# Optimization experiments

Hardware: AMD Instinct MI355X
Metric: run time of the kernel (lower is better)

## Reference

```python
import jax, jax.numpy as jnp
import numpy as np

NEG = -1e30  # safe -inf surrogate (keeps grads finite)
BLANK = 0
PRIOR_SCALE = 0.3


def prior_logsumexp(log_probs, input_lengths):
    # log_probs: [T, N, V]; logsumexp over all valid (t, n) frames -> [1, V]
    T = log_probs.shape[0]
    mask = jnp.arange(T)[:, None] < input_lengths[None, :]  # [T, N]
    masked = jnp.where(mask[:, :, None], log_probs, NEG)
    return jax.nn.logsumexp(masked, axis=(0, 1))[None, :]


def ctc_loss_mean(log_probs, targets, input_lengths, target_lengths):
    # Exact CTC forward (alpha) recursion, vectorized over batch, scanned over time.
    # log_probs: [T, N, V] (log scores), targets: [N, S] with values >= 1.
    T, N, V = log_probs.shape
    S = targets.shape[1]
    L = 2 * S + 1  # extended label sequence with interleaved blanks
    ext = jnp.full((N, L), BLANK, dtype=targets.dtype).at[:, 1::2].set(targets)
    # skip transition j-2 -> j allowed iff ext[j] != blank and ext[j] != ext[j-2]
    skip = jnp.zeros((N, L), bool).at[:, 2:].set(
        (ext[:, 2:] != BLANK) & (ext[:, 2:] != ext[:, :-2]))
    pad1 = jnp.full((N, 1), NEG, log_probs.dtype)
    pad2 = jnp.full((N, 2), NEG, log_probs.dtype)

    e0 = jnp.take_along_axis(log_probs[0], ext, axis=1)  # [N, L]
    alpha0 = (jnp.full((N, L), NEG, log_probs.dtype)
              .at[:, 0].set(e0[:, 0])
              .at[:, 1].set(e0[:, 1]))

    def step(alpha, xs):
        lp_t, t = xs
        emit = jnp.take_along_axis(lp_t, ext, axis=1)  # [N, L]
        s1 = jnp.concatenate([pad1, alpha[:, :-1]], axis=1)
        s2 = jnp.where(skip, jnp.concatenate([pad2, alpha[:, :-2]], axis=1), NEG)
        new = jax.nn.logsumexp(jnp.stack([alpha, s1, s2], 0), axis=0) + emit
        # freeze finished utterances (t >= input_length)
        alpha = jnp.where((t < input_lengths)[:, None], new, alpha)
        return alpha, None

    alpha, _ = jax.lax.scan(step, alpha0, (log_probs[1:], jnp.arange(1, T)))

    i1 = (2 * target_lengths)[:, None]
    a1 = jnp.take_along_axis(alpha, i1, axis=1)[:, 0]
    a2 = jnp.take_along_axis(alpha, i1 - 1, axis=1)[:, 0]
    ll = jnp.logaddexp(a1, a2)  # total log-likelihood per utterance
    # k2.ctc_loss(reduction='mean', target_lengths=...) == mean of (-ll / target_len)
    return jnp.mean(-ll / target_lengths.astype(log_probs.dtype))


def setup_inputs() -> dict:
    key = jax.random.key(0)
    k1, k2, k3, k4, k5 = jax.random.split(key, 5)
    T, N, V, S = 2000, 32, 256, 256
    log_probs = jax.nn.log_softmax(jax.random.normal(k1, (T, N, V), jnp.float32), axis=-1)
    log_priors = jax.nn.log_softmax(0.5 * jax.random.normal(k2, (1, V), jnp.float32), axis=-1)
    targets = jax.random.randint(k3, (N, S), 1, V)          # non-blank labels
    input_lengths = jax.random.randint(k4, (N,), T // 2, T + 1)
    target_lengths = jax.random.randint(k5, (N,), S // 2, S + 1)
    return {"log_probs": log_probs, "log_priors": log_priors, "targets": targets,
            "input_lengths": input_lengths, "target_lengths": target_lengths}


def reference(log_probs, log_priors, targets, input_lengths, target_lengths):
    # (1) detached label-prior accumulation pass (as in training step)
    log_batch_priors_sum = jax.lax.stop_gradient(prior_logsumexp(log_probs, input_lengths))
    # (2) prior-scaled log probs (log_priors broadcasts [1,V] -> [T,N,V])
    scaled = log_probs - PRIOR_SCALE * log_priors
    # (3) CTC forward-backward loss
    loss = ctc_loss_mean(scaled, targets, input_lengths, target_lengths)
    return loss, log_batch_priors_sum
```

## Files before the change

kernel.cpp:

```cpp
#include <hip/hip_runtime.h>

#define PRIOR_SCALE 0.3f
#define NEGF (-1e30f)
#define LOG2E_F 1.4426950408889634f
#define LN2_F 0.6931471805599453f
#define K_SS 8
#define MARG 24

#define PHASE_BARRIER() \
  asm volatile("s_waitcnt lgkmcnt(0)\n\ts_barrier" ::: "memory")

__device__ __forceinline__ float fexp2(float x) { return __builtin_amdgcn_exp2f(x); }
__device__ __forceinline__ float flog2(float x) { return __builtin_amdgcn_logf(x); }

__device__ __forceinline__ float lse2b(float a, float b) {
  float m = fmaxf(a, b);
  float d = fminf(a, b) - m;
  return m + flog2(1.0f + fexp2(d));
}

__device__ __forceinline__ float shr1_dpp(float x, float fill) {
  return __int_as_float(__builtin_amdgcn_update_dpp(
      __float_as_int(fill), __float_as_int(x), 0x138 , 0xF, 0xF, false));
}
__device__ __forceinline__ int shr1_dpp_i(int x, int fill) {
  return __builtin_amdgcn_update_dpp(fill, x, 0x138, 0xF, 0xF, false);
}
template <int CTRL, int RM>
__device__ __forceinline__ int dppi(int x) {
  return __builtin_amdgcn_update_dpp(x, x, CTRL, RM, 0xF, false);
}
__device__ __forceinline__ int imax2(int a, int b) { return a > b ? a : b; }

__device__ __forceinline__ void issue_pair(float& e, float& b, uint32_t offE,
                                           uint32_t offB, uint64_t base) {
  asm volatile("global_load_dword %0, %2, %4\n\t"
               "global_load_dword %1, %3, %4"
               : "=v"(e), "=v"(b)
               : "v"(offE), "v"(offB), "s"(base));
}
__device__ __forceinline__ void wait_pair(float& e, float& b) {
  asm volatile("s_waitcnt vmcnt(14)" : "+v"(e), "+v"(b));
}

extern "C" __global__ void __launch_bounds__(256, 1)
ctc_fused_kernel(const float* __restrict__ lp, const float* __restrict__ lpri,
                 const int* __restrict__ tgt, const int* __restrict__ ilen,
                 const int* __restrict__ tlen, float* __restrict__ nll,
                 float* __restrict__ partial, int pblocks,
                 int T, int N, int V, int S) {
  if ((int)blockIdx.x >= N) {
    const int pb = blockIdx.x - N;
    const int v = threadIdx.x;
    float s = 0.0f;
    for (int t = pb; t < T; t += pblocks) {
      const float* base = lp + (size_t)t * N * V + v;
      for (int nn = 0; nn < N; ++nn) {
        float x = base[(size_t)nn * V];
        s += (t < ilen[nn]) ? __expf(x) : 0.0f;
      }
    }
    partial[(size_t)pb * V + v] = s;
    return;
  }

  const int n = blockIdx.x;
  const int g = threadIdx.x;
  const int lane = g & 63;
  const int wid = __builtin_amdgcn_readfirstlane(threadIdx.x >> 6);
  __shared__ __align__(16) float mb[3][2048];
  __shared__ int mbe[3][256];
  __shared__ float afin[513];

  const int len = __builtin_amdgcn_readfirstlane(ilen[n]);
  const int tl = tlen[n];

  const int* trow = tgt + n * S;
  const int tv = trow[g];
  const int tvp = (g > 0) ? trow[g - 1] : -1;
  const float skf = (g > 0 && tv != tvp) ? 1.0f : 0.0f;
  const float ep1 = (-PRIOR_SCALE * lpri[tv]) * LOG2E_F;
  const float epb = (-PRIOR_SCALE * lpri[0]) * LOG2E_F;
  const int penB = MARG * ((lane & 15) + 1);
  const int penC = MARG * ((lane & 31) + 1);

  const float* rp = lp + (size_t)n * V;
  const uint32_t RBu = (uint32_t)(N * V * 4);
  const uint32_t tvb = (uint32_t)tv * 4u;
  const uint64_t gbase = (uint64_t)(uintptr_t)rp;

  float x0 = 0.0f, x1 = 0.0f, x2 = 0.0f;
  int e = 0;
  { float b0 = rp[0], e0 = rp[tv];
    if (g == 0) {
      x0 = fexp2(fmaf(b0, LOG2E_F, epb));
      x1 = fexp2(fmaf(e0, LOG2E_F, ep1));
    } }
  for (int idx = g; idx < 3 * 2048; idx += 256) ((float*)mb)[idx] = 0.0f;
  for (int idx = g; idx < 3 * 256; idx += 256) ((int*)mbe)[idx] = 0;

  float eR0, eR1, eR2, eR3, eR4, eR5, eR6, eR7;
  float bR0, bR1, bR2, bR3, bR4, bR5, bR6, bR7;
#define PRO(K) { uint32_t tt = (uint32_t)((1 + K < len) ? (1 + K) : (len - 1)); \
                 issue_pair(eR##K, bR##K, tt * RBu + tvb, tt * RBu, gbase); }
  PRO(0) PRO(1) PRO(2) PRO(3) PRO(4) PRO(5) PRO(6) PRO(7)
#undef PRO
  uint32_t ofB;
  { uint32_t tn = (uint32_t)((1 + K_SS < len) ? (1 + K_SS) : (len - 1));
    ofB = tn * RBu; }

  float mv0 = 0, mv1 = 0, mv2 = 0, mv3 = 0, mv4 = 0, mv5 = 0, mv6 = 0, mv7 = 0;

  PHASE_BARRIER();

  const int nss = (len - 1 + K_SS - 1) / K_SS;
  const int P = nss + 3;

#define STEP(KK, T_, DSC_) {                                                   \
    const int t = (T_);                                                        \
    if (t < len) {                                                             \
      wait_pair(eR##KK, bR##KK);                                               \
      float e1  = fexp2(fmaf(eR##KK, LOG2E_F, ep1));                           \
      float ebl = fexp2(fmaf(bR##KK, LOG2E_F, epb));                           \
      issue_pair(eR##KK, bR##KK, ofB + tvb, ofB, gbase);                       \
      ofB += ((t + 1 + K_SS) < len) ? RBu : 0u;                                \
      float am1 = ldexpf(shr1_dpp(x1, mv##KK), (DSC_));                        \
      am1 = fminf(am1, 1.0e33f);                         \
      float sel = (g == 255) ? x1 : 0.0f;                                      \
      float y0 = (x0 + am1) * ebl;                                             \
      float y1 = fmaf(skf, am1, x1 + x0) * e1;                                 \
      x2 = (x2 + sel) * ebl;                                                   \
      x0 = y0; x1 = y1;                                                        \
      if (lane == 63 && wid < 3) mb[wid][t] = y1;       \
    } }

  for (int p = 0; p < P; ++p) {
    const int i = p - wid;
    if (i >= 0 && i < nss) {
      const int t0 = 1 + i * K_SS;
      int eA = 0, eB = 0;
      if (wid > 0) {
        eB = mbe[wid - 1][i];
        eA = (i > 0) ? mbe[wid - 1][i - 1] : eB;
        const float4* mrow = (const float4*)&mb[wid - 1][t0 - 1];
        float4 q0 = mrow[0], q1 = mrow[1];
        mv0 = q0.x; mv1 = q0.y; mv2 = q0.z; mv3 = q0.w;
        mv4 = q1.x; mv5 = q1.y; mv6 = q1.z; mv7 = q1.w;
      }
      int dscL, dsc0;
      {
        float mxv = fmaxf(fmaxf(x0, x1), x2);
        int ex = (int)((__float_as_uint(mxv) >> 23) & 0xFFu) - 127;
        int ecand = (mxv > 0.0f) ? (e + ex - 40) : -2000000;
        if (wid > 0 && lane == 0) ecand = imax2(ecand, imax2(eA, eB) - MARG);
        int v = ecand;
        v = imax2(v, dppi<0x111, 0xF>(v) - MARG);
        v = imax2(v, dppi<0x112, 0xF>(v) - 2 * MARG);
        v = imax2(v, dppi<0x114, 0xF>(v) - 4 * MARG);
        v = imax2(v, dppi<0x118, 0xF>(v) - 8 * MARG);
        v = imax2(v, dppi<0x142, 0xA>(v) - penB);
        v = imax2(v, dppi<0x143, 0xC>(v) - penC);
        int dsc = e - v;
        x0 = ldexpf(x0, dsc);
        x1 = ldexpf(x1, dsc);
        x2 = ldexpf(x2, dsc);
        e = v;
        if (lane == 63 && wid < 3) mbe[wid][i] = e;
        int eprevL = shr1_dpp_i(e, eB);
        dscL = eprevL - e;
        dsc0 = (lane == 0) ? (eA - e) : dscL;
      }
      STEP(0, t0 + 0, dsc0)  STEP(1, t0 + 1, dscL)
      STEP(2, t0 + 2, dscL)  STEP(3, t0 + 3, dscL)
      STEP(4, t0 + 4, dscL)  STEP(5, t0 + 5, dscL)
      STEP(6, t0 + 6, dscL)  STEP(7, t0 + 7, dscL)
    }
    PHASE_BARRIER();
  }
#undef STEP

  asm volatile("s_waitcnt vmcnt(0)");
  asm volatile("" :: "v"(eR0), "v"(eR1), "v"(eR2), "v"(eR3),
                     "v"(eR4), "v"(eR5), "v"(eR6), "v"(eR7));
  asm volatile("" :: "v"(bR0), "v"(bR1), "v"(bR2), "v"(bR3),
                     "v"(bR4), "v"(bR5), "v"(bR6), "v"(bR7));

  const float ef = (float)e;
  afin[2 * g]     = fmaxf(flog2(x0) + ef, NEGF);
  afin[2 * g + 1] = fmaxf(flog2(x1) + ef, NEGF);
  if (g == 255) afin[512] = fmaxf(flog2(x2) + ef, NEGF);
  __syncthreads();
  if (g == 0) {
    const int i1 = 2 * tl;
    float ll = lse2b(afin[i1], afin[i1 - 1]) * LN2_F;
    nll[n] = -ll / (float)tl;
  }
}

extern "C" __global__ void __launch_bounds__(256)
finalize1_kernel(const float* __restrict__ partial, int nstripes,
                 float* __restrict__ partial2) {
  const int v = threadIdx.x;
  const int b = blockIdx.x;
  float s = 0.0f;
  for (int pb = b; pb < nstripes; pb += 32) s += partial[(size_t)pb * 256 + v];
  partial2[(size_t)b * 256 + v] = s;
}
extern "C" __global__ void __launch_bounds__(256)
finalize2_kernel(const float* __restrict__ partial2, const float* __restrict__ nll,
                 float* __restrict__ out, int N) {
  const int v = threadIdx.x;
  float s = 0.0f;
#pragma unroll
  for (int b = 0; b < 32; ++b) s += partial2[(size_t)b * 256 + v];
  out[1 + v] = __logf(s);
  if (v == 0) {
    float acc = 0.0f;
#pragma unroll 8
    for (int i = 0; i < N; ++i) acc += nll[i];
    out[0] = acc / (float)N;
  }
}

extern "C" __global__ void finalize_kernel(const float* __restrict__ partial, int nstripes,
                                           const float* __restrict__ nll,
                                           float* __restrict__ out, int N, int V) {
  const int v = threadIdx.x;
  float s = 0.0f;
#pragma unroll 4
  for (int pb = 0; pb < nstripes; ++pb) s += partial[(size_t)pb * V + v];
  out[1 + v] = __logf(s);
  if (v == 0) {
    float acc = 0.0f;
#pragma unroll 8
    for (int i = 0; i < N; ++i) acc += nll[i];
    out[0] = acc / (float)N;
  }
}

extern "C" void kernel_launch(void* const* d_in, const int* in_sizes, int n_in,
                              void* d_out, int out_size, void* d_ws, size_t ws_size,
                              hipStream_t stream) {
  const float* lp   = (const float*)d_in[0];
  const float* lpri = (const float*)d_in[1];
  const int*   tgt  = (const int*)d_in[2];
  const int*   ilen = (const int*)d_in[3];
  const int*   tlen = (const int*)d_in[4];
  const int V = in_sizes[1];
  const int N = in_sizes[3];
  const int S = in_sizes[2] / N;
  const int T = in_sizes[0] / (N * V);

  int pblocks = 200;
  size_t need2stage = ((size_t)pblocks * V + 32 * 256 + 64) * sizeof(float);
  size_t need1stage = ((size_t)pblocks * V + 64) * sizeof(float);

  float* out = (float*)d_out;

  if (ws_size >= need2stage) {
    float* partial  = (float*)d_ws;
    float* partial2 = partial + (size_t)pblocks * V;
    float* nll      = partial2 + 32 * 256;
    ctc_fused_kernel<<<N + pblocks, 256, 0, stream>>>(lp, lpri, tgt, ilen, tlen,
                                                      nll, partial, pblocks, T, N, V, S);
    finalize1_kernel<<<32, 256, 0, stream>>>(partial, pblocks, partial2);
    finalize2_kernel<<<1, 256, 0, stream>>>(partial2, nll, out, N);
  } else {
    if (ws_size < need1stage) {
      long avail = (long)(ws_size / sizeof(float)) - 64;
      pblocks = (int)(avail / V);
      if (pblocks < 1) pblocks = 1;
    }
    float* partial = (float*)d_ws;
    float* nll = partial + (size_t)pblocks * V;
    ctc_fused_kernel<<<N + pblocks, 256, 0, stream>>>(lp, lpri, tgt, ilen, tlen,
                                                      nll, partial, pblocks, T, N, V, S);
    finalize_kernel<<<1, 256, 0, stream>>>(partial, pblocks, nll, out, N, V);
  }
}
```

Before: 213.2 us.

## Double superstep length to halve barriers, decouple prefetch ring depth

Raises the superstep from 8 to 16 timesteps per wavefront phase, so each wave runs twice as many recursion steps between block barriers and rescaling passes. The global-load prefetch ring stays 8 deep and is now indexed separately from the superstep length. The exponent headroom for rescaling grows from 40 to 60 to cover the longer gap between rescales. The cost is more registers for the neighbour-boundary values, longer pipeline fill and drain across the 4-wave wavefront, and more risk of float overflow or underflow between rescales.

```diff
diff --git a/kernel.cpp b/kernel.cpp
--- a/kernel.cpp
+++ b/kernel.cpp
@@ -4,8 +4,10 @@
 #define NEGF (-1e30f)
 #define LOG2E_F 1.4426950408889634f
 #define LN2_F 0.6931471805599453f
-#define K_SS 8
+#define K_SS 16
+#define RING_D 8
 #define MARG 24
+#define PEG 60
 
 #define PHASE_BARRIER() \
   asm volatile("s_waitcnt lgkmcnt(0)\n\ts_barrier" ::: "memory")
@@ -69,7 +71,7 @@
   const int lane = g & 63;
   const int wid = __builtin_amdgcn_readfirstlane(threadIdx.x >> 6);
   __shared__ __align__(16) float mb[3][2048];
-  __shared__ int mbe[3][256];
+  __shared__ int mbe[3][128];
   __shared__ float afin[513];
 
   const int len = __builtin_amdgcn_readfirstlane(ilen[n]);
@@ -97,7 +99,7 @@
       x1 = fexp2(fmaf(e0, LOG2E_F, ep1));
     } }
   for (int idx = g; idx < 3 * 2048; idx += 256) ((float*)mb)[idx] = 0.0f;
-  for (int idx = g; idx < 3 * 256; idx += 256) ((int*)mbe)[idx] = 0;
+  if (g < 3 * 128) ((int*)mbe)[g] = 0;
 
   float eR0, eR1, eR2, eR3, eR4, eR5, eR6, eR7;
   float bR0, bR1, bR2, bR3, bR4, bR5, bR6, bR7;
@@ -106,25 +108,26 @@
   PRO(0) PRO(1) PRO(2) PRO(3) PRO(4) PRO(5) PRO(6) PRO(7)
 #undef PRO
   uint32_t ofB;
-  { uint32_t tn = (uint32_t)((1 + K_SS < len) ? (1 + K_SS) : (len - 1));
+  { uint32_t tn = (uint32_t)((1 + RING_D < len) ? (1 + RING_D) : (len - 1));
     ofB = tn * RBu; }
 
-  float mv0 = 0, mv1 = 0, mv2 = 0, mv3 = 0, mv4 = 0, mv5 = 0, mv6 = 0, mv7 = 0;
+  float mv0 = 0, mv1 = 0, mv2 = 0, mv3 = 0, mv4 = 0, mv5 = 0, mv6 = 0, mv7 = 0,
+        mv8 = 0, mv9 = 0, mv10 = 0, mv11 = 0, mv12 = 0, mv13 = 0, mv14 = 0, mv15 = 0;
 
   PHASE_BARRIER();
 
   const int nss = (len - 1 + K_SS - 1) / K_SS;
   const int P = nss + 3;
 
-#define STEP(KK, T_, DSC_) {                                                   \
+#define STEP(KK, MVK, T_, DSC_) {                                              \
     const int t = (T_);                                                        \
     if (t < len) {                                                             \
       wait_pair(eR##KK, bR##KK);                                               \
       float e1  = fexp2(fmaf(eR##KK, LOG2E_F, ep1));                           \
       float ebl = fexp2(fmaf(bR##KK, LOG2E_F, epb));                           \
       issue_pair(eR##KK, bR##KK, ofB + tvb, ofB, gbase);                       \
-      ofB += ((t + 1 + K_SS) < len) ? RBu : 0u;                                \
-      float am1 = ldexpf(shr1_dpp(x1, mv##KK), (DSC_));                        \
+      ofB += ((t + 1 + RING_D) < len) ? RBu : 0u;                              \
+      float am1 = ldexpf(shr1_dpp(x1, mv##MVK), (DSC_));                       \
       am1 = fminf(am1, 1.0e33f);                         \
       float sel = (g == 255) ? x1 : 0.0f;                                      \
       float y0 = (x0 + am1) * ebl;                                             \
@@ -143,15 +146,17 @@
         eB = mbe[wid - 1][i];
         eA = (i > 0) ? mbe[wid - 1][i - 1] : eB;
         const float4* mrow = (const float4*)&mb[wid - 1][t0 - 1];
-        float4 q0 = mrow[0], q1 = mrow[1];
-        mv0 = q0.x; mv1 = q0.y; mv2 = q0.z; mv3 = q0.w;
-        mv4 = q1.x; mv5 = q1.y; mv6 = q1.z; mv7 = q1.w;
+        float4 q0 = mrow[0], q1 = mrow[1], q2 = mrow[2], q3 = mrow[3];
+        mv0 = q0.x;  mv1 = q0.y;  mv2 = q0.z;  mv3 = q0.w;
+        mv4 = q1.x;  mv5 = q1.y;  mv6 = q1.z;  mv7 = q1.w;
+        mv8 = q2.x;  mv9 = q2.y;  mv10 = q2.z; mv11 = q2.w;
+        mv12 = q3.x; mv13 = q3.y; mv14 = q3.z; mv15 = q3.w;
       }
       int dscL, dsc0;
       {
         float mxv = fmaxf(fmaxf(x0, x1), x2);
         int ex = (int)((__float_as_uint(mxv) >> 23) & 0xFFu) - 127;
-        int ecand = (mxv > 0.0f) ? (e + ex - 40) : -2000000;
+        int ecand = (mxv > 0.0f) ? (e + ex - PEG) : -2000000;
         if (wid > 0 && lane == 0) ecand = imax2(ecand, imax2(eA, eB) - MARG);
         int v = ecand;
         v = imax2(v, dppi<0x111, 0xF>(v) - MARG);
@@ -170,10 +175,14 @@
         dscL = eprevL - e;
         dsc0 = (lane == 0) ? (eA - e) : dscL;
       }
-      STEP(0, t0 + 0, dsc0)  STEP(1, t0 + 1, dscL)
-      STEP(2, t0 + 2, dscL)  STEP(3, t0 + 3, dscL)
-      STEP(4, t0 + 4, dscL)  STEP(5, t0 + 5, dscL)
-      STEP(6, t0 + 6, dscL)  STEP(7, t0 + 7, dscL)
+      STEP(0, 0, t0 + 0, dsc0)    STEP(1, 1, t0 + 1, dscL)
+      STEP(2, 2, t0 + 2, dscL)    STEP(3, 3, t0 + 3, dscL)
+      STEP(4, 4, t0 + 4, dscL)    STEP(5, 5, t0 + 5, dscL)
+      STEP(6, 6, t0 + 6, dscL)    STEP(7, 7, t0 + 7, dscL)
+      STEP(0, 8, t0 + 8, dscL)    STEP(1, 9, t0 + 9, dscL)
+      STEP(2, 10, t0 + 10, dscL)  STEP(3, 11, t0 + 11, dscL)
+      STEP(4, 12, t0 + 12, dscL)  STEP(5, 13, t0 + 13, dscL)
+      STEP(6, 14, t0 + 14, dscL)  STEP(7, 15, t0 + 15, dscL)
     }
     PHASE_BARRIER();
   }
```

New measurement: 185.9 us. -12.8%, faster.
